# Optimization experiments

Measured on AMD Instinct MI355X. Metric: run time of the kernel, lower is better.

Reference implementation:

```python
import jax, jax.numpy as jnp
import numpy as np

N_HEAD = 8


def _axial_attn(x, wq, wk, wv, fw, fb, axis):
    # x: (B, T, H, W, C); axis is the axial axis in (B, nh, T, H, W, d): 2=T, 3=H, 4=W
    B, T, H, W, C = x.shape
    d = C // N_HEAD

    def heads(y):
        # (B,T,H,W,C) -> (B, nh, T, H, W, d)
        return jnp.moveaxis(y.reshape(B, T, H, W, N_HEAD, d), -2, 1)

    q, k, v = heads(x @ wq), heads(x @ wk), heads(x @ wv)
    # restrict attention to the axial axis: move it to -2, all other dims are batch
    q = jnp.moveaxis(q, axis, -2)
    k = jnp.moveaxis(k, axis, -2)
    v = jnp.moveaxis(v, axis, -2)
    scale = 1.0 / jnp.sqrt(jnp.asarray(d, x.dtype))
    scores = jnp.einsum('...ld,...md->...lm', q * scale, k)
    att = jax.nn.softmax(scores, axis=-1)
    o = jnp.einsum('...lm,...md->...ld', att, v)
    o = jnp.moveaxis(o, -2, axis)            # restore axial axis position
    o = jnp.moveaxis(o, 1, -2).reshape(B, T, H, W, C)  # merge heads
    return o @ fw + fb


def setup_inputs() -> dict:
    key = jax.random.key(0)
    ks = jax.random.split(key, 16)
    C = 512
    x = jax.random.normal(ks[0], (4, C, 16, 32, 32), jnp.float32)
    s = 0.02

    def w(k):
        return jax.random.normal(k, (C, C), jnp.float32) * s

    inp = {'x': x}
    i = 1
    for ax in ('w', 'h', 't'):
        inp[f'wq_{ax}'] = w(ks[i])
        inp[f'wk_{ax}'] = w(ks[i + 1])
        inp[f'wv_{ax}'] = w(ks[i + 2])
        inp[f'fc_{ax}'] = w(ks[i + 3])
        inp[f'fb_{ax}'] = jnp.zeros((C,), jnp.float32)
        i += 4
    return inp


def reference(x, wq_w, wk_w, wv_w, fc_w, fb_w,
              wq_h, wk_h, wv_h, fc_h, fb_h,
              wq_t, wk_t, wv_t, fc_t, fb_t):
    xt = jnp.moveaxis(x, 1, -1)  # (B, C, T, H, W) -> (B, T, H, W, C)
    out = (_axial_attn(xt, wq_w, wk_w, wv_w, fc_w, fb_w, 4)   # attend along W
           + _axial_attn(xt, wq_h, wk_h, wv_h, fc_h, fb_h, 3)  # attend along H
           + _axial_attn(xt, wq_t, wk_t, wv_t, fc_t, fb_t, 2))  # attend along T
    return jnp.moveaxis(out, -1, 1)  # back to (B, C, T, H, W)
```

## Files before the change

kernel.cpp:

```cpp
#include <hip/hip_runtime.h>
#include <stdint.h>

typedef __attribute__((ext_vector_type(8))) short bf16x8;
typedef __attribute__((ext_vector_type(4))) float f32x4;

static __device__ __forceinline__ short f2bf(float f) {
  uint32_t u = __builtin_bit_cast(uint32_t, f);
  u += 0x7fffu + ((u >> 16) & 1u);
  return (short)(u >> 16);
}

static __device__ __forceinline__ void gload_lds16(const void* g, void* l) {
  __builtin_amdgcn_global_load_lds((const __attribute__((address_space(1))) void*)g,
                                   (__attribute__((address_space(3))) void*)l, 16, 0, 0);
}

#define GFENCE asm volatile("" ::: "memory")

__global__ __launch_bounds__(256) void transpose_x_k(const float* __restrict__ x,
                                                     short* __restrict__ xb) {
  __shared__ float t[64][65];
  const int pt = blockIdx.x, ct = blockIdx.y, b = blockIdx.z;
  const int tid = threadIdx.x;
#pragma unroll
  for (int i = 0; i < 16; i++) {
    int cc = i * 4 + (tid >> 6);
    int pp = tid & 63;
    t[cc][pp] = x[(size_t)(b * 512 + ct * 64 + cc) * 16384 + pt * 64 + pp];
  }
  __syncthreads();
#pragma unroll
  for (int i = 0; i < 2; i++) {
    int seg = i * 256 + tid;
    int pw = seg >> 3, c8 = seg & 7;
    short tmp[8];
#pragma unroll
    for (int k = 0; k < 8; k++) tmp[k] = f2bf(t[c8 * 8 + k][pw]);
    *(uint4*)&xb[(size_t)(b * 16384 + pt * 64 + pw) * 512 + ct * 64 + c8 * 8] =
        *(const uint4*)tmp;
  }
}

struct WPtrs {
  const float* src[12];
  short* dst[12];
  int ld[12];
};

__global__ __launch_bounds__(256) void transpose_w_k(WPtrs P) {
  __shared__ float t[64][65];
  const int kt = blockIdx.x, nt = blockIdx.y, z = blockIdx.z;
  const float* src = P.src[z];
  short* dst = P.dst[z];
  const int ld = P.ld[z];
  const int tid = threadIdx.x;
#pragma unroll
  for (int i = 0; i < 16; i++) {
    int kk = i * 4 + (tid >> 6);
    int nn = tid & 63;
    t[kk][nn] = src[(kt * 64 + kk) * 512 + nt * 64 + nn];
  }
  __syncthreads();
#pragma unroll
  for (int i = 0; i < 2; i++) {
    int seg = i * 256 + tid;
    int nn = seg >> 3, k8 = seg & 7;
    short tmp[8];
#pragma unroll
    for (int k = 0; k < 8; k++) tmp[k] = f2bf(t[k8 * 8 + k][nn]);
    *(uint4*)&dst[(size_t)(nt * 64 + nn) * ld + kt * 64 + k8 * 8] = *(const uint4*)tmp;
  }
}

__global__ void bsum_k(const float* a, const float* b, const float* c, float* o) {
  int i = blockIdx.x * 256 + threadIdx.x;
  if (i < 512) o[i] = a[i] + b[i] + c[i];
}

#define LOADB(q)                                                               \
  do {                                                                         \
    _Pragma("unroll") for (int ni = 0; ni < 4; ++ni) bfr[ni] =                 \
        *(const bf16x8*)(smem + (q) * 32768 + 16384 + boff + ni * 1024);       \
  } while (0)

#define LOADA(q, mq)                                                           \
  do {                                                                         \
    _Pragma("unroll") for (int mi = 0; mi < 4; ++mi) af[mi] =                  \
        *(const bf16x8*)(smem + (q) * 32768 + aoff + ((mq) * 4 + mi) * 1024);  \
  } while (0)

#define MFMA16(mq)                                                             \
  do {                                                                         \
    __builtin_amdgcn_s_setprio(1);                                             \
    _Pragma("unroll") for (int mi = 0; mi < 4; ++mi)                           \
        _Pragma("unroll") for (int ni = 0; ni < 4; ++ni) acc[(mq) * 4 + mi]    \
            [ni] = __builtin_amdgcn_mfma_f32_16x16x32_bf16(                    \
                af[mi], bfr[ni], acc[(mq) * 4 + mi][ni], 0, 0, 0);             \
    __builtin_amdgcn_s_setprio(0);                                             \
    GFENCE;                                                                    \
  } while (0)

#define PH0(q, SA)                                                             \
  do {                                                                         \
    LOADB(q);                                                                  \
    LOADA(q, 0);                                                               \
    SA;                                                                        \
    GFENCE;                                                                    \
    __builtin_amdgcn_s_barrier();                                              \
    asm volatile("s_waitcnt lgkmcnt(0)" ::: "memory");                         \
    __builtin_amdgcn_sched_barrier(0);                                         \
    MFMA16(0);                                                                 \
    GFENCE;                                                                    \
    __builtin_amdgcn_s_barrier();                                              \
    GFENCE;                                                                    \
  } while (0)

#define PH1(q, SB, VM)                                                         \
  do {                                                                         \
    LOADA(q, 1);                                                               \
    SB;                                                                        \
    VM;                                                                        \
    GFENCE;                                                                    \
    __builtin_amdgcn_s_barrier();                                              \
    asm volatile("s_waitcnt lgkmcnt(0)" ::: "memory");                         \
    __builtin_amdgcn_sched_barrier(0);                                         \
    MFMA16(1);                                                                 \
    GFENCE;                                                                    \
    __builtin_amdgcn_s_barrier();                                              \
    GFENCE;                                                                    \
  } while (0)

#define VM8 asm volatile("s_waitcnt vmcnt(8)" ::: "memory")
#define VM4 asm volatile("s_waitcnt vmcnt(4)" ::: "memory")
#define VM0 asm volatile("s_waitcnt vmcnt(0)" ::: "memory")

template <int MODE>
__global__ __launch_bounds__(512, 2) void gemm256_k(const short* __restrict__ A,
                                                    int lda,
                                                    const short* __restrict__ B,
                                                    int ldb, void* __restrict__ Dp,
                                                    int K, int ldd,
                                                    const float* __restrict__ bsum,
                                                    int GN) {
  extern __shared__ char smem[];
  const int tid = threadIdx.x;
  const int lane = tid & 63, wave = tid >> 6;
  const int wr = wave >> 2, wc = wave & 3;
  const int r4 = lane & 15, kl = lane >> 4;

  int bid = blockIdx.x;
  const int cpx = gridDim.x >> 3;
  bid = (bid & 7) * cpx + (bid >> 3);
  int bm, bn;
  if constexpr (MODE == 0) {
    bn = bid % GN;
    bm = bid / GN;
  } else {
    bm = bid & 1;
    bn = bid >> 1;
  }

  const int NT = K >> 5;

  const int srow = tid >> 2;
  const int schk = (tid & 3) ^ ((tid >> 4) & 3);
  const short* gA0 = A + (size_t)(bm * 256 + srow) * lda + schk * 8;
  const short* gB0 = B + (size_t)(bn * 256 + srow) * ldb + schk * 8;

  auto stage = [&](int tt, int x) {
    const short* g = x ? gB0 : gA0;
    const size_t rstep = (size_t)128 * (x ? ldb : lda);
    const size_t koff = (size_t)tt * 32;
    char* ldst = smem + (tt & 3) * 32768 + x * 16384 + wave * 1024;
#pragma unroll
    for (int i = 0; i < 2; ++i)
      gload_lds16(g + i * rstep + koff, ldst + i * 8192);
  };

  const int kls = kl ^ (r4 >> 2);
  const int aoff = wr * 8192 + r4 * 64 + kls * 16;
  const int boff = wc * 4096 + r4 * 64 + kls * 16;

  f32x4 acc[8][4];
#pragma unroll
  for (int i = 0; i < 8; ++i)
#pragma unroll
    for (int j = 0; j < 4; ++j) acc[i][j] = (f32x4){0.f, 0.f, 0.f, 0.f};
  bf16x8 af[4], bfr[4];

  stage(0, 0);
  stage(0, 1);
  stage(1, 0);
  stage(1, 1);
  stage(2, 0);
  stage(2, 1);
  VM8;
  GFENCE;
  __builtin_amdgcn_s_barrier();
  GFENCE;

  int t = 0;
  for (; t < NT - 3; ++t) {
    const int q = t & 3;
    PH0(q, stage(t + 3, 0));
    PH1(q, stage(t + 3, 1), VM8);
  }
  {
    const int q = t & 3;
    PH0(q, (void)0);
    PH1(q, (void)0, VM4);
    ++t;
  }
  {
    const int q = t & 3;
    PH0(q, (void)0);
    PH1(q, (void)0, VM0);
    ++t;
  }
  {
    const int q = t & 3;
    PH0(q, (void)0);
    PH1(q, (void)0, (void)0);
  }

  const int m0 = wr * 128 + kl * 4;
  const int n0 = wc * 64 + r4;
  if (MODE == 0) {
    short* D = (short*)Dp;
#pragma unroll
    for (int mi = 0; mi < 8; ++mi)
#pragma unroll
      for (int ni = 0; ni < 4; ++ni)
#pragma unroll
        for (int r = 0; r < 4; ++r) {
          int row = bm * 256 + m0 + mi * 16 + r;
          int col = bn * 256 + n0 + ni * 16;
          D[(size_t)row * ldd + col] = f2bf(acc[mi][ni][r]);
        }
  } else {
    float* D = (float*)Dp + (size_t)((bn * 256) >> 14) * 8388608;
#pragma unroll
    for (int mi = 0; mi < 8; ++mi)
#pragma unroll
      for (int ni = 0; ni < 4; ++ni)
#pragma unroll
        for (int r = 0; r < 4; ++r) {
          int c = bm * 256 + m0 + mi * 16 + r;
          int n = (bn * 256 + n0 + ni * 16) & 16383;
          if (MODE == 1)
            D[(size_t)c * 16384 + n] = acc[mi][ni][r] + bsum[c];
          else
            D[(size_t)c * 16384 + n] += acc[mi][ni][r];
        }
  }
}

template <int L>
__global__ __launch_bounds__(256) void attn_k(const short* __restrict__ qkv,
                                              short* __restrict__ o, int Adiv, int Bmul,
                                              int Cmul, int stride, int obase,
                                              int ostride) {
  constexpr int R = 256 / L;
  constexpr int SPT = (L * L) / 256;
  constexpr int OPT = 64 / R;
  __shared__ short Ks[L][72];
  __shared__ short Vs[L][72];
  __shared__ short Qs[L][72];
  __shared__ float att[L][L + 1];
  const int tid = threadIdx.x;
  const int blk = blockIdx.x;
  const int s = blk >> 3, head = blk & 7;
  const int base = (s / Adiv) * Bmul + (s % Adiv) * Cmul;

  for (int idx = tid; idx < L * 8 * 3; idx += 256) {
    int part = idx / (L * 8);
    int rem = idx - part * (L * 8);
    int row = rem >> 3, seg = rem & 7;
    int n = base + row * stride;
    uint4 v = *(const uint4*)&qkv[(size_t)n * 1536 + part * 512 + head * 64 + seg * 8];
    short* dst = (part == 0 ? &Qs[row][0] : part == 1 ? &Ks[row][0] : &Vs[row][0]);
    *(uint4*)(dst + seg * 8) = v;
  }
  __syncthreads();

  const int l = tid / R, r = tid % R;
  float q[64];
#pragma unroll
  for (int w = 0; w < 8; w++) {
    uint4 u = *(const uint4*)&Qs[l][w * 8];
    uint32_t arr[4] = {u.x, u.y, u.z, u.w};
#pragma unroll
    for (int p = 0; p < 4; p++) {
      q[w * 8 + p * 2] = __builtin_bit_cast(float, arr[p] << 16);
      q[w * 8 + p * 2 + 1] = __builtin_bit_cast(float, arr[p] & 0xffff0000u);
    }
  }
  float sc[SPT];
#pragma unroll
  for (int jj = 0; jj < SPT; jj++) {
    int j = jj * R + r;
    float a0 = 0.f;
#pragma unroll
    for (int w = 0; w < 8; w++) {
      uint4 u = *(const uint4*)&Ks[j][w * 8];
      uint32_t arr[4] = {u.x, u.y, u.z, u.w};
#pragma unroll
      for (int p = 0; p < 4; p++) {
        a0 += q[w * 8 + p * 2] * __builtin_bit_cast(float, arr[p] << 16);
        a0 += q[w * 8 + p * 2 + 1] * __builtin_bit_cast(float, arr[p] & 0xffff0000u);
      }
    }
    sc[jj] = a0 * 0.125f;
  }
  float mx = sc[0];
#pragma unroll
  for (int jj = 1; jj < SPT; jj++) mx = fmaxf(mx, sc[jj]);
#pragma unroll
  for (int d = 1; d < R; d <<= 1) mx = fmaxf(mx, __shfl_xor(mx, d));
  float p_[SPT];
  float sum = 0.f;
#pragma unroll
  for (int jj = 0; jj < SPT; jj++) {
    p_[jj] = __expf(sc[jj] - mx);
    sum += p_[jj];
  }
#pragma unroll
  for (int d = 1; d < R; d <<= 1) sum += __shfl_xor(sum, d);
  float inv = 1.0f / sum;
#pragma unroll
  for (int jj = 0; jj < SPT; jj++) att[l][jj * R + r] = p_[jj] * inv;
  __syncthreads();

  float oa[OPT] = {};
#pragma unroll 4
  for (int j = 0; j < L; j++) {
    float a = att[l][j];
    if constexpr (OPT == 8) {
      uint4 u = *(const uint4*)&Vs[j][r * 8];
      uint32_t arr[4] = {u.x, u.y, u.z, u.w};
#pragma unroll
      for (int p = 0; p < 4; p++) {
        oa[p * 2] += a * __builtin_bit_cast(float, arr[p] << 16);
        oa[p * 2 + 1] += a * __builtin_bit_cast(float, arr[p] & 0xffff0000u);
      }
    } else {
      uint2 u = *(const uint2*)&Vs[j][r * 4];
      uint32_t arr[2] = {u.x, u.y};
#pragma unroll
      for (int p = 0; p < 2; p++) {
        oa[p * 2] += a * __builtin_bit_cast(float, arr[p] << 16);
        oa[p * 2 + 1] += a * __builtin_bit_cast(float, arr[p] & 0xffff0000u);
      }
    }
  }
  short tmp[OPT];
#pragma unroll
  for (int i = 0; i < OPT; i++) tmp[i] = f2bf(oa[i]);
  int n = base + l * stride;
  if constexpr (OPT == 8)
    *(uint4*)&o[(size_t)n * ostride + obase + head * 64 + r * 8] = *(const uint4*)tmp;
  else
    *(uint2*)&o[(size_t)n * ostride + obase + head * 64 + r * 4] = *(const uint2*)tmp;
}

extern "C" void kernel_launch(void* const* d_in, const int* in_sizes, int n_in,
                              void* d_out, int out_size, void* d_ws, size_t ws_size,
                              hipStream_t stream) {
  const float* x = (const float*)d_in[0];
  const float* wq[3];
  const float* wk[3];
  const float* wv[3];
  const float* fc[3];
  const float* fb[3];
  for (int a = 0; a < 3; a++) {
    wq[a] = (const float*)d_in[1 + a * 5];
    wk[a] = (const float*)d_in[2 + a * 5];
    wv[a] = (const float*)d_in[3 + a * 5];
    fc[a] = (const float*)d_in[4 + a * 5];
    fb[a] = (const float*)d_in[5 + a * 5];
  }
  char* ws = (char*)d_ws;
  short* xb = (short*)(ws);
  short* qkv = (short*)(ws + 67108864);
  short* wqkvt = (short*)(ws + 268435456);
  short* fctA = (short*)(ws + 273154048);
  float* bsum = (float*)(ws + 274726912);
  short* ob = (short*)(ws + 274728960);
  float* out = (float*)d_out;

  const bool fused = ws_size >= 476055552ull;

  (void)hipFuncSetAttribute((const void*)&gemm256_k<0>,
                            hipFuncAttributeMaxDynamicSharedMemorySize, 131072);
  (void)hipFuncSetAttribute((const void*)&gemm256_k<1>,
                            hipFuncAttributeMaxDynamicSharedMemorySize, 131072);
  (void)hipFuncSetAttribute((const void*)&gemm256_k<2>,
                            hipFuncAttributeMaxDynamicSharedMemorySize, 131072);

  WPtrs P;
  for (int a = 0; a < 3; a++) {
    P.src[a * 4 + 0] = wq[a];
    P.src[a * 4 + 1] = wk[a];
    P.src[a * 4 + 2] = wv[a];
    P.src[a * 4 + 3] = fc[a];
    P.dst[a * 4 + 0] = wqkvt + (size_t)a * 1536 * 512;
    P.dst[a * 4 + 1] = wqkvt + (size_t)a * 1536 * 512 + 512 * 512;
    P.dst[a * 4 + 2] = wqkvt + (size_t)a * 1536 * 512 + 2 * 512 * 512;
    P.dst[a * 4 + 3] = fctA + a * 512;
    P.ld[a * 4 + 0] = 512;
    P.ld[a * 4 + 1] = 512;
    P.ld[a * 4 + 2] = 512;
    P.ld[a * 4 + 3] = 1536;
  }
  transpose_w_k<<<dim3(8, 8, 12), 256, 0, stream>>>(P);
  bsum_k<<<dim3(2), 256, 0, stream>>>(fb[0], fb[1], fb[2], bsum);
  transpose_x_k<<<dim3(256, 8, 4), 256, 0, stream>>>(x, xb);

  const int Ad[3] = {1, 32, 1024};
  const int Bm_[3] = {32, 1024, 16384};
  const int Cm[3] = {0, 1, 1};
  const int St[3] = {1, 32, 1024};
  const int Ls[3] = {32, 32, 16};

  for (int a = 0; a < 3; a++) {
    gemm256_k<0><<<dim3(1536), 512, 131072, stream>>>(
        xb, 512, wqkvt + (size_t)a * 1536 * 512, 512, (void*)qkv, 512, 1536,
        nullptr, 6);
    const int obase = fused ? a * 512 : 0;
    const int ostr = fused ? 1536 : 512;
    if (Ls[a] == 32)
      attn_k<32><<<dim3(2048 * 8), 256, 0, stream>>>(qkv, ob, Ad[a], Bm_[a], Cm[a],
                                                     St[a], obase, ostr);
    else
      attn_k<16><<<dim3(4096 * 8), 256, 0, stream>>>(qkv, ob, Ad[a], Bm_[a], Cm[a],
                                                     St[a], obase, ostr);
    if (!fused) {
      if (a == 0)
        gemm256_k<1><<<dim3(512), 512, 131072, stream>>>(
            fctA + a * 512, 1536, ob, 512, (void*)out, 512, 0, bsum, 0);
      else
        gemm256_k<2><<<dim3(512), 512, 131072, stream>>>(
            fctA + a * 512, 1536, ob, 512, (void*)out, 512, 0, bsum, 0);
    }
  }
  if (fused) {
    gemm256_k<1><<<dim3(512), 512, 131072, stream>>>(
        fctA, 1536, ob, 1536, (void*)out, 1536, 0, bsum, 0);
  }
}
```

Before: 843.0 us.

## Replace 256x256 GEMM tile with 128x128 tile, 3-stage static-LDS pipeline

The 512-thread 256x256-tile GEMM, which used 128KB of dynamic LDS and a 4-buffer two-phase pipeline, is replaced by a 256-thread 128x128-tile kernel. The new kernel uses 48KB of static LDS with 3 stages and a simpler single-phase body, and is launched with four times as many blocks. The aim is better occupancy and less barrier and scheduling complexity. In exchange, each block gets less operand reuse, so global and L2 traffic per FLOP goes up.

Result: slower. 893.6 us (+6.0%).

```diff
diff --git a/kernel.cpp b/kernel.cpp
--- a/kernel.cpp
+++ b/kernel.cpp
@@ -77,75 +77,18 @@
   if (i < 512) o[i] = a[i] + b[i] + c[i];
 }
 
-#define LOADB(q)                                                               \
-  do {                                                                         \
-    _Pragma("unroll") for (int ni = 0; ni < 4; ++ni) bfr[ni] =                 \
-        *(const bf16x8*)(smem + (q) * 32768 + 16384 + boff + ni * 1024);       \
-  } while (0)
-
-#define LOADA(q, mq)                                                           \
-  do {                                                                         \
-    _Pragma("unroll") for (int mi = 0; mi < 4; ++mi) af[mi] =                  \
-        *(const bf16x8*)(smem + (q) * 32768 + aoff + ((mq) * 4 + mi) * 1024);  \
-  } while (0)
-
-#define MFMA16(mq)                                                             \
-  do {                                                                         \
-    __builtin_amdgcn_s_setprio(1);                                             \
-    _Pragma("unroll") for (int mi = 0; mi < 4; ++mi)                           \
-        _Pragma("unroll") for (int ni = 0; ni < 4; ++ni) acc[(mq) * 4 + mi]    \
-            [ni] = __builtin_amdgcn_mfma_f32_16x16x32_bf16(                    \
-                af[mi], bfr[ni], acc[(mq) * 4 + mi][ni], 0, 0, 0);             \
-    __builtin_amdgcn_s_setprio(0);                                             \
-    GFENCE;                                                                    \
-  } while (0)
-
-#define PH0(q, SA)                                                             \
-  do {                                                                         \
-    LOADB(q);                                                                  \
-    LOADA(q, 0);                                                               \
-    SA;                                                                        \
-    GFENCE;                                                                    \
-    __builtin_amdgcn_s_barrier();                                              \
-    asm volatile("s_waitcnt lgkmcnt(0)" ::: "memory");                         \
-    __builtin_amdgcn_sched_barrier(0);                                         \
-    MFMA16(0);                                                                 \
-    GFENCE;                                                                    \
-    __builtin_amdgcn_s_barrier();                                              \
-    GFENCE;                                                                    \
-  } while (0)
-
-#define PH1(q, SB, VM)                                                         \
-  do {                                                                         \
-    LOADA(q, 1);                                                               \
-    SB;                                                                        \
-    VM;                                                                        \
-    GFENCE;                                                                    \
-    __builtin_amdgcn_s_barrier();                                              \
-    asm volatile("s_waitcnt lgkmcnt(0)" ::: "memory");                         \
-    __builtin_amdgcn_sched_barrier(0);                                         \
-    MFMA16(1);                                                                 \
-    GFENCE;                                                                    \
-    __builtin_amdgcn_s_barrier();                                              \
-    GFENCE;                                                                    \
-  } while (0)
-
-#define VM8 asm volatile("s_waitcnt vmcnt(8)" ::: "memory")
-#define VM4 asm volatile("s_waitcnt vmcnt(4)" ::: "memory")
-#define VM0 asm volatile("s_waitcnt vmcnt(0)" ::: "memory")
-
 template <int MODE>
-__global__ __launch_bounds__(512, 2) void gemm256_k(const short* __restrict__ A,
+__global__ __launch_bounds__(256, 3) void gemm128_k(const short* __restrict__ A,
                                                     int lda,
                                                     const short* __restrict__ B,
                                                     int ldb, void* __restrict__ Dp,
                                                     int K, int ldd,
                                                     const float* __restrict__ bsum,
                                                     int GN) {
-  extern __shared__ char smem[];
+  __shared__ char smem[49152];
   const int tid = threadIdx.x;
   const int lane = tid & 63, wave = tid >> 6;
-  const int wr = wave >> 2, wc = wave & 3;
+  const int wm = (wave >> 1) << 6, wn = (wave & 1) << 6;
   const int r4 = lane & 15, kl = lane >> 4;
 
   int bid = blockIdx.x;
@@ -156,97 +99,107 @@
     bn = bid % GN;
     bm = bid / GN;
   } else {
-    bm = bid & 1;
-    bn = bid >> 1;
+    bm = bid & 3;
+    bn = bid >> 2;
   }
 
   const int NT = K >> 5;
 
-  const int srow = tid >> 2;
-  const int schk = (tid & 3) ^ ((tid >> 4) & 3);
-  const short* gA0 = A + (size_t)(bm * 256 + srow) * lda + schk * 8;
-  const short* gB0 = B + (size_t)(bn * 256 + srow) * ldb + schk * 8;
-
-  auto stage = [&](int tt, int x) {
-    const short* g = x ? gB0 : gA0;
-    const size_t rstep = (size_t)128 * (x ? ldb : lda);
+  const int schk = (lane & 3) ^ ((lane >> 3) & 3);
+  const short* gA0 = A + (size_t)(bm * 128 + wave * 32 + (lane >> 2)) * lda + schk * 8;
+  const short* gB0 = B + (size_t)(bn * 128 + wave * 32 + (lane >> 2)) * ldb + schk * 8;
+  char* lA0 = smem + wave * 2048;
+
+  auto stage = [&](int tt, int qq) {
     const size_t koff = (size_t)tt * 32;
-    char* ldst = smem + (tt & 3) * 32768 + x * 16384 + wave * 1024;
-#pragma unroll
-    for (int i = 0; i < 2; ++i)
-      gload_lds16(g + i * rstep + koff, ldst + i * 8192);
+    char* d = lA0 + qq * 16384;
+    gload_lds16(gA0 + koff, d);
+    gload_lds16(gA0 + (size_t)16 * lda + koff, d + 1024);
+    gload_lds16(gB0 + koff, d + 8192);
+    gload_lds16(gB0 + (size_t)16 * ldb + koff, d + 9216);
   };
 
-  const int kls = kl ^ (r4 >> 2);
-  const int aoff = wr * 8192 + r4 * 64 + kls * 16;
-  const int boff = wc * 4096 + r4 * 64 + kls * 16;
-
-  f32x4 acc[8][4];
-#pragma unroll
-  for (int i = 0; i < 8; ++i)
+  const int kls = kl ^ ((r4 >> 1) & 3);
+  const int aoff = (wm + r4) * 64 + kls * 16;
+  const int boff = 8192 + (wn + r4) * 64 + kls * 16;
+
+  f32x4 acc[4][4];
+#pragma unroll
+  for (int i = 0; i < 4; ++i)
 #pragma unroll
     for (int j = 0; j < 4; ++j) acc[i][j] = (f32x4){0.f, 0.f, 0.f, 0.f};
-  bf16x8 af[4], bfr[4];
+
+#define BODY(q)                                                                \
+  do {                                                                         \
+    __builtin_amdgcn_s_barrier();                                              \
+    bf16x8 af[4], bfr[4];                                                      \
+    _Pragma("unroll") for (int mi = 0; mi < 4; ++mi) af[mi] =                  \
+        *(const bf16x8*)(smem + (q) * 16384 + aoff + mi * 1024);               \
+    _Pragma("unroll") for (int ni = 0; ni < 4; ++ni) bfr[ni] =                 \
+        *(const bf16x8*)(smem + (q) * 16384 + boff + ni * 1024);               \
+    __builtin_amdgcn_s_setprio(1);                                             \
+    _Pragma("unroll") for (int mi = 0; mi < 4; ++mi)                           \
+        _Pragma("unroll") for (int ni = 0; ni < 4; ++ni) acc[mi][ni] =         \
+            __builtin_amdgcn_mfma_f32_16x16x32_bf16(af[mi], bfr[ni],           \
+                                                    acc[mi][ni], 0, 0, 0);     \
+    __builtin_amdgcn_s_setprio(0);                                             \
+    __builtin_amdgcn_s_barrier();                                              \
+    GFENCE;                                                                    \
+  } while (0)
+
+#define VM8 asm volatile("s_waitcnt vmcnt(8)" ::: "memory")
+#define VM4 asm volatile("s_waitcnt vmcnt(4)" ::: "memory")
+#define VM0 asm volatile("s_waitcnt vmcnt(0)" ::: "memory")
 
   stage(0, 0);
-  stage(0, 1);
-  stage(1, 0);
   stage(1, 1);
-  stage(2, 0);
-  stage(2, 1);
+  stage(2, 2);
+
+  int t = 0, q = 0;
+  for (; t < NT - 3; ++t) {
+    VM8;
+    BODY(q);
+    stage(t + 3, q);
+    q = (q == 2) ? 0 : q + 1;
+  }
   VM8;
-  GFENCE;
-  __builtin_amdgcn_s_barrier();
-  GFENCE;
-
-  int t = 0;
-  for (; t < NT - 3; ++t) {
-    const int q = t & 3;
-    PH0(q, stage(t + 3, 0));
-    PH1(q, stage(t + 3, 1), VM8);
-  }
-  {
-    const int q = t & 3;
-    PH0(q, (void)0);
-    PH1(q, (void)0, VM4);
-    ++t;
-  }
-  {
-    const int q = t & 3;
-    PH0(q, (void)0);
-    PH1(q, (void)0, VM0);
-    ++t;
-  }
-  {
-    const int q = t & 3;
-    PH0(q, (void)0);
-    PH1(q, (void)0, (void)0);
-  }
-
-  const int m0 = wr * 128 + kl * 4;
-  const int n0 = wc * 64 + r4;
+  BODY(q);
+  q = (q == 2) ? 0 : q + 1;
+  VM4;
+  BODY(q);
+  q = (q == 2) ? 0 : q + 1;
+  VM0;
+  BODY(q);
+
+#undef BODY
+#undef VM8
+#undef VM4
+#undef VM0
+
+  const int m0 = wm + kl * 4;
+  const int n0 = wn + r4;
   if (MODE == 0) {
     short* D = (short*)Dp;
 #pragma unroll
-    for (int mi = 0; mi < 8; ++mi)
+    for (int mi = 0; mi < 4; ++mi)
 #pragma unroll
       for (int ni = 0; ni < 4; ++ni)
 #pragma unroll
         for (int r = 0; r < 4; ++r) {
-          int row = bm * 256 + m0 + mi * 16 + r;
-          int col = bn * 256 + n0 + ni * 16;
+          int row = bm * 128 + m0 + mi * 16 + r;
+          int col = bn * 128 + n0 + ni * 16;
           D[(size_t)row * ldd + col] = f2bf(acc[mi][ni][r]);
         }
   } else {
-    float* D = (float*)Dp + (size_t)((bn * 256) >> 14) * 8388608;
-#pragma unroll
-    for (int mi = 0; mi < 8; ++mi)
+    float* D = (float*)Dp + (size_t)((bn * 128) >> 14) * 8388608;
+#pragma unroll
+    for (int mi = 0; mi < 4; ++mi)
 #pragma unroll
       for (int ni = 0; ni < 4; ++ni)
 #pragma unroll
         for (int r = 0; r < 4; ++r) {
-          int c = bm * 256 + m0 + mi * 16 + r;
-          int n = (bn * 256 + n0 + ni * 16) & 16383;
+          int c = bm * 128 + m0 + mi * 16 + r;
+          int n = (bn * 128 + n0 + ni * 16) & 16383;
           if (MODE == 1)
             D[(size_t)c * 16384 + n] = acc[mi][ni][r] + bsum[c];
           else
@@ -390,13 +343,6 @@
 
   const bool fused = ws_size >= 476055552ull;
 
-  (void)hipFuncSetAttribute((const void*)&gemm256_k<0>,
-                            hipFuncAttributeMaxDynamicSharedMemorySize, 131072);
-  (void)hipFuncSetAttribute((const void*)&gemm256_k<1>,
-                            hipFuncAttributeMaxDynamicSharedMemorySize, 131072);
-  (void)hipFuncSetAttribute((const void*)&gemm256_k<2>,
-                            hipFuncAttributeMaxDynamicSharedMemorySize, 131072);
-
   WPtrs P;
   for (int a = 0; a < 3; a++) {
     P.src[a * 4 + 0] = wq[a];
@@ -423,9 +369,9 @@
   const int Ls[3] = {32, 32, 16};
 
   for (int a = 0; a < 3; a++) {
-    gemm256_k<0><<<dim3(1536), 512, 131072, stream>>>(
+    gemm128_k<0><<<dim3(6144), 256, 0, stream>>>(
         xb, 512, wqkvt + (size_t)a * 1536 * 512, 512, (void*)qkv, 512, 1536,
-        nullptr, 6);
+        nullptr, 12);
     const int obase = fused ? a * 512 : 0;
     const int ostr = fused ? 1536 : 512;
     if (Ls[a] == 32)
@@ -436,15 +382,15 @@
                                                      St[a], obase, ostr);
     if (!fused) {
       if (a == 0)
-        gemm256_k<1><<<dim3(512), 512, 131072, stream>>>(
+        gemm128_k<1><<<dim3(2048), 256, 0, stream>>>(
             fctA + a * 512, 1536, ob, 512, (void*)out, 512, 0, bsum, 0);
       else
-        gemm256_k<2><<<dim3(512), 512, 131072, stream>>>(
+        gemm128_k<2><<<dim3(2048), 256, 0, stream>>>(
             fctA + a * 512, 1536, ob, 512, (void*)out, 512, 0, bsum, 0);
     }
   }
   if (fused) {
-    gemm256_k<1><<<dim3(512), 512, 131072, stream>>>(
+    gemm128_k<1><<<dim3(2048), 256, 0, stream>>>(
         fctA, 1536, ob, 1536, (void*)out, 1536, 0, bsum, 0);
   }
 }
```
